# Optimization experiments

Measured on AMD Instinct MI355X. Metric: run time of the kernel, lower is better.

## Reference

```python
import jax, jax.numpy as jnp
import numpy as np

DIM = 512
HID = 2048
E = 16
B = 8
N = 2048
THRESHOLD = 0.8
CAP_FACTOR = 2.0  # eval mode
MIN_EXPERT_CAPACITY = 4
LOSS_COEF = 0.01
CAP = max(MIN_EXPERT_CAPACITY, min(N, int(N * CAP_FACTOR / E)))  # 256


def setup_inputs() -> dict:
    key = jax.random.key(0)
    k1, k2, k3, k4 = jax.random.split(key, 4)
    x = jax.random.normal(k1, (B, N, DIM), dtype=jnp.float32)
    w_gating = jax.random.normal(k2, (DIM, E), dtype=jnp.float32)
    std1 = 1.0 / np.sqrt(HID)
    std2 = 1.0 / np.sqrt(DIM)
    w1 = jax.random.uniform(k3, (E, DIM, HID), jnp.float32, -std1, std1)
    w2 = jax.random.uniform(k4, (E, HID, DIM), jnp.float32, -std2, std2)
    return {"x": x, "w_gating": w_gating, "w1": w1, "w2": w2}


def _gate(x, w_gating):
    # raw gate probabilities [B, N, E]
    raw = jax.nn.softmax(jnp.einsum('bnd,de->bne', x, w_gating), axis=-1)
    order = jnp.argsort(-raw, axis=-1)                      # descending sort indices
    sp = jnp.take_along_axis(raw, order, axis=-1)           # sorted probs (desc)
    cum = jnp.cumsum(sp, axis=-1)
    tm = cum >= THRESHOLD
    k = jnp.argmax(tm.astype(jnp.float32), axis=-1) + 1     # dynamic k per token
    k = jnp.where(jnp.any(tm, axis=-1), k, E)
    # select top-k in sorted order, renormalize
    rank = jnp.arange(E)
    sel = (rank < k[..., None]).astype(raw.dtype)           # [B,N,E] sorted order
    selp = sp * sel
    normp = selp / jnp.sum(selp, axis=-1, keepdims=True)
    # scatter back to expert order via inverse permutation
    inv = jnp.argsort(order, axis=-1)
    mask = jnp.take_along_axis(sel, inv, axis=-1)           # expert_masks [B,N,E]
    weights = jnp.take_along_axis(normp, inv, axis=-1)      # expert_weights
    # capacity: exclusive cumsum over tokens
    pos = (jnp.cumsum(mask, axis=-2) - mask) * mask
    mask = mask * (pos < float(CAP)).astype(mask.dtype)
    pos = pos * mask
    pos_tok = jnp.sum(pos, axis=-1).astype(jnp.int32)       # [B,N] (summed across experts, as in source)
    in_cap = (pos_tok < CAP).astype(raw.dtype)
    oh = jax.nn.one_hot(pos_tok, CAP, dtype=raw.dtype) * in_cap[..., None]  # [B,N,CAP]
    dispatch = mask[..., None] * oh[..., None, :]           # [B,N,E,CAP]
    combine = (weights * mask)[..., None] * oh[..., None, :]
    density = jnp.mean(mask, axis=-2)
    density_proxy = jnp.mean(raw, axis=-2)
    loss = jnp.mean(density_proxy * density) * float(E * E)
    loss = loss + 0.0 * jnp.mean(k.astype(jnp.float32))
    return dispatch, combine, loss


def reference(x, w_gating, w1, w2):
    dispatch, combine, loss = _gate(x, w_gating)
    expert_inputs = jnp.einsum('bnd,bnec->ebcd', x, dispatch)        # [E,B,CAP,D]
    ei = expert_inputs.reshape(E, B * CAP, DIM)
    hidden = jax.nn.gelu(jnp.einsum('end,edh->enh', ei, w1), approximate=False)
    eo = jnp.einsum('enh,ehd->end', hidden, w2).reshape(E, B, CAP, DIM)
    output = jnp.einsum('ebcd,bnec->bnd', eo, combine)               # [B,N,D]
    return output, loss * LOSS_COEF
```

## Files before the change

kernel.cpp:

```cpp
#include <hip/hip_runtime.h>
#include <math.h>

#define DIMC 512
#define HIDC 2048
#define EC   16
#define BC   8
#define NC   2048
#define CAPC 256
#define BN   (BC * NC)
#define THRESH 0.8f

typedef unsigned short u16;
typedef __attribute__((ext_vector_type(8))) __bf16 bf16x8;
typedef __attribute__((ext_vector_type(4))) float f32x4;

__device__ __forceinline__ float bf2f(unsigned u) {
    union { unsigned i; float f; } v; v.i = u << 16; return v.f;
}
__device__ __forceinline__ u16 f2bf(float f) {
    union { float f; unsigned i; } v; v.f = f;
    unsigned r = v.i + 0x7fff + ((v.i >> 16) & 1);
    return (u16)(r >> 16);
}
__device__ __forceinline__ float gelu_f(float x) {
    float u = 0.7978845608028654f * (x + 0.044715f * x * x * x);
    float t = __expf(2.f * u);
    float th = 1.f - 2.f / (t + 1.f);
    return 0.5f * x * (1.f + th);
}

__global__ void init_kernel(int* __restrict__ heads, int* __restrict__ pos_tok)
{
    int i = blockIdx.x * 256 + threadIdx.x;
    if (i < EC * BC * CAPC) heads[i] = -1;
    if (i < BN) pos_tok[i] = 0;
}

__global__ __launch_bounds__(256) void gate_kernel(const float* __restrict__ x,
                                                   const float* __restrict__ wg,
                                                   float* __restrict__ raw,
                                                   float* __restrict__ weights,
                                                   float* __restrict__ maskf)
{
    __shared__ float wlds[16][516];
    __shared__ float lg[16][16];
    int t = threadIdx.x;
    int tok16 = t >> 4, e = t & 15;
    int token = blockIdx.x * 16 + tok16;

    {
        const float4* wg4 = (const float4*)wg;
#pragma unroll
        for (int j = 0; j < 8; ++j) {
            int idx4 = j * 256 + t;
            float4 v = wg4[idx4];
            int d  = idx4 >> 2;
            int e0 = (idx4 & 3) * 4;
            wlds[e0 + 0][d] = v.x;
            wlds[e0 + 1][d] = v.y;
            wlds[e0 + 2][d] = v.z;
            wlds[e0 + 3][d] = v.w;
        }
    }
    __syncthreads();

    const float4* xr = (const float4*)(x + (size_t)token * DIMC);
    const float4* wl = (const float4*)&wlds[e][0];
    float a0 = 0.f, a1 = 0.f, a2 = 0.f, a3 = 0.f;
#pragma unroll 4
    for (int i = 0; i < 128; i += 4) {
        float4 xa = xr[i], xb = xr[i+1], xc = xr[i+2], xd = xr[i+3];
        float4 wa = wl[i], wb = wl[i+1], wc = wl[i+2], wd = wl[i+3];
        a0 = fmaf(xa.w, wa.w, fmaf(xa.z, wa.z, fmaf(xa.y, wa.y, fmaf(xa.x, wa.x, a0))));
        a1 = fmaf(xb.w, wb.w, fmaf(xb.z, wb.z, fmaf(xb.y, wb.y, fmaf(xb.x, wb.x, a1))));
        a2 = fmaf(xc.w, wc.w, fmaf(xc.z, wc.z, fmaf(xc.y, wc.y, fmaf(xc.x, wc.x, a2))));
        a3 = fmaf(xd.w, wd.w, fmaf(xd.z, wd.z, fmaf(xd.y, wd.y, fmaf(xd.x, wd.x, a3))));
    }
    float logit = (a0 + a1) + (a2 + a3);

    float m = logit;
#pragma unroll
    for (int off = 8; off >= 1; off >>= 1) m = fmaxf(m, __shfl_xor(m, off, 16));
    float p = expf(logit - m);
    float s = p;
#pragma unroll
    for (int off = 8; off >= 1; off >>= 1) s += __shfl_xor(s, off, 16);
    p = p / s;

    int rank = 0;
    float cum = p;
#pragma unroll
    for (int j = 1; j < 16; ++j) {
        float op = __shfl_xor(p, j, 16);
        int oidx = e ^ j;
        bool ahead = (op > p) || (op == p && oidx < e);
        if (ahead) { rank++; cum += op; }
    }
    bool tm = (cum >= THRESH);
    int kr = tm ? rank : (EC - 1);
#pragma unroll
    for (int off = 8; off >= 1; off >>= 1) kr = min(kr, __shfl_xor(kr, off, 16));
    bool sel = (rank <= kr);

    float dsel = sel ? p : 0.f;
    float denom = dsel;
#pragma unroll
    for (int off = 8; off >= 1; off >>= 1) denom += __shfl_xor(denom, off, 16);
    float w = sel ? (p / denom) : 0.f;

    size_t o = (size_t)token * EC + e;
    raw[o]     = p;
    weights[o] = w;
    maskf[o]   = sel ? 1.f : 0.f;
    (void)lg;
}

__global__ __launch_bounds__(64) void capacity_kernel(const float* __restrict__ raw,
                                                      float* __restrict__ maskf,
                                                      int* __restrict__ pos,
                                                      int* __restrict__ pos_tok,
                                                      float* __restrict__ density,
                                                      float* __restrict__ proxy)
{
    int t = blockIdx.x;
    int b = t / EC, e = t % EC;
    int lane = threadIdx.x;

    size_t idx = ((size_t)b * NC + lane) * EC + e;
    const size_t step = (size_t)64 * EC;
    float mv = maskf[idx];
    float rv = raw[idx];

    int count = 0;
    float rsum = 0.f;
    for (int n0 = 0; n0 < NC; n0 += 64) {
        float mn = 0.f, rn = 0.f;
        if (n0 + 64 < NC) { mn = maskf[idx + step]; rn = raw[idx + step]; }

        rsum += rv;
        unsigned long long bal = __ballot(mv != 0.f);
        int below = __popcll(bal & ((1ull << lane) - 1ull));
        int pval = 0;
        if (mv != 0.f) {
            pval = count + below;
            if (pval >= CAPC) { maskf[idx] = 0.f; pval = 0; }
            else if (pval > 0) atomicAdd(&pos_tok[b * NC + n0 + lane], pval);
        }
        pos[idx] = pval;
        count += __popcll(bal);

        idx += step; mv = mn; rv = rn;
    }
#pragma unroll
    for (int off = 32; off >= 1; off >>= 1) rsum += __shfl_xor(rsum, off);
    if (lane == 0) {
        int admitted = count < CAPC ? count : CAPC;
        density[t] = (float)admitted / (float)NC;
        proxy[t]   = rsum / (float)NC;
    }
}

__global__ __launch_bounds__(256) void build_kernel(const float* __restrict__ maskf,
                                                    const int* __restrict__ pos,
                                                    const int* __restrict__ pos_tok,
                                                    int* __restrict__ heads,
                                                    int* __restrict__ nxt,
                                                    int* __restrict__ node_tok)
{
    int id = blockIdx.x * 256 + threadIdx.x;
    int token = id >> 4, e = id & 15;
    if (maskf[id] == 0.f) return;
    int c = pos_tok[token];
    if (c >= CAPC) return;
    int b = token >> 11;
    int slot = (e * BC + b) * CAPC + c;
    int node = (e * BC + b) * CAPC + pos[id];
    node_tok[node] = token;
    nxt[node] = atomicExch(&heads[slot], node);
}

__global__ __launch_bounds__(256) void gather_ei_kernel(const float* __restrict__ x,
                                                        const int* __restrict__ heads,
                                                        const int* __restrict__ nxt,
                                                        const int* __restrict__ node_tok,
                                                        u16* __restrict__ ei)
{
    int slot = blockIdx.x * 4 + (threadIdx.x >> 6);
    int lane = threadIdx.x & 63;
    float a[8] = {0,0,0,0,0,0,0,0};
    int node = heads[slot];
    while (node >= 0) {
        const float4* xr = (const float4*)(x + (size_t)node_tok[node] * DIMC) + lane * 2;
        float4 v0 = xr[0], v1 = xr[1];
        a[0]+=v0.x; a[1]+=v0.y; a[2]+=v0.z; a[3]+=v0.w;
        a[4]+=v1.x; a[5]+=v1.y; a[6]+=v1.z; a[7]+=v1.w;
        node = nxt[node];
    }
    uint4 v;
    v.x = (unsigned)f2bf(a[0]) | ((unsigned)f2bf(a[1]) << 16);
    v.y = (unsigned)f2bf(a[2]) | ((unsigned)f2bf(a[3]) << 16);
    v.z = (unsigned)f2bf(a[4]) | ((unsigned)f2bf(a[5]) << 16);
    v.w = (unsigned)f2bf(a[6]) | ((unsigned)f2bf(a[7]) << 16);
    *(uint4*)(ei + (size_t)slot * DIMC + lane * 8) = v;
}

__global__ __launch_bounds__(256) void transpose_cvt_all_kernel(const float* __restrict__ w1,
                                                                const float* __restrict__ w2,
                                                                u16* __restrict__ w1t,
                                                                u16* __restrict__ w2t)
{
    __shared__ float tile[64][65];
    int bid = blockIdx.x;
    const float* in; u16* out; int R, C, bx, by, e;
    if (bid < 4096) {
        e = bid >> 8; int r = bid & 255;
        bx = r & 31; by = r >> 5;
        in = w1; out = w1t; R = DIMC; C = HIDC;
    } else {
        bid -= 4096;
        e = bid >> 8; int r = bid & 255;
        bx = r & 7;  by = r >> 3;
        in = w2; out = w2t; R = HIDC; C = DIMC;
    }
    size_t eoff = (size_t)e * R * C;
    int c0 = bx * 64, r0 = by * 64;
    int tid = threadIdx.x;
    int rr = tid >> 4;
    int cc = (tid & 15) * 4;
#pragma unroll
    for (int i = 0; i < 4; ++i) {
        float4 v = *(const float4*)(in + eoff + (size_t)(r0 + rr + 16 * i) * C + c0 + cc);
        tile[rr + 16 * i][cc + 0] = v.x;
        tile[rr + 16 * i][cc + 1] = v.y;
        tile[rr + 16 * i][cc + 2] = v.z;
        tile[rr + 16 * i][cc + 3] = v.w;
    }
    __syncthreads();
    int c = tid >> 2;
    int r8 = (tid & 3) * 16;
    u16 buf[16];
#pragma unroll
    for (int j = 0; j < 16; ++j) buf[j] = f2bf(tile[r8 + j][c]);
    u16* op = out + eoff + (size_t)(c0 + c) * R + r0 + r8;
    *(uint4*)(op)     = *(uint4*)&buf[0];
    *(uint4*)(op + 8) = *(uint4*)&buf[8];
}

__device__ __forceinline__ void async_cp16(const u16* g, u16* l) {
    __builtin_amdgcn_global_load_lds(
        (const __attribute__((address_space(1))) unsigned*)g,
        (__attribute__((address_space(3))) unsigned*)l, 16, 0, 0);
}

#define GFENCE() asm volatile("" ::: "memory")
#define BAR() do { GFENCE(); __builtin_amdgcn_s_barrier(); GFENCE(); } while (0)

__device__ __forceinline__ int xcd_swz(int id, int nwg) {
    int chunk = nwg >> 3;
    return (id & 7) * chunk + (id >> 3);
}

template<int GELU>
__global__ __launch_bounds__(512, 2) void gemm256_kernel(
    const u16* __restrict__ A, const u16* __restrict__ Bt, u16* __restrict__ C,
    int M, int N, int K, long sA, long sB, long sC)
{
    __shared__ __align__(16) u16 lds[2][2][2][8192];
    const int bxc = N >> 8, byc = M >> 8;
    int swzid = xcd_swz(blockIdx.x, gridDim.x);
    const int e  = swzid / (bxc * byc);
    int rr2 = swzid % (bxc * byc);
    const int bm = (rr2 / bxc) * 256, bn = (rr2 % bxc) * 256;
    const int t = threadIdx.x, lane = t & 63, w = t >> 6;
    const int wm = w & 1;
    const int wn = w >> 1;
    const int bh = wn >> 1;
    const int q = lane >> 4, m16 = lane & 15;

    const u16* g[2][2][2];
    int lofs[2];
#pragma unroll
    for (int j = 0; j < 2; ++j) {
        int l = j * 512 + t, r = l >> 3, c = (l & 7) ^ (r & 7);
        lofs[j] = l * 8;
        g[0][0][j] = A  + (size_t)e * sA + (size_t)(bm + r) * K + c * 8;
        g[0][1][j] = A  + (size_t)e * sA + (size_t)(bm + 128 + r) * K + c * 8;
        g[1][0][j] = Bt + (size_t)e * sB + (size_t)(bn + r) * K + c * 8;
        g[1][1][j] = Bt + (size_t)e * sB + (size_t)(bn + 128 + r) * K + c * 8;
    }

    int aro[8], bro[4];
#pragma unroll
    for (int mt = 0; mt < 8; ++mt) {
        int r = mt * 16 + m16;
        aro[mt] = r * 64 + (q ^ (r & 7)) * 8;
    }
#pragma unroll
    for (int nt = 0; nt < 4; ++nt) {
        int r = (wn & 1) * 64 + nt * 16 + m16;
        bro[nt] = r * 64 + (q ^ (r & 7)) * 8;
    }

    auto STAGE = [&](int buf, int op, int half) {
#pragma unroll
        for (int j = 0; j < 2; ++j) {
            async_cp16(g[op][half][j], &lds[buf][op][half][lofs[j]]);
            g[op][half][j] += 64;
        }
    };

    const int nk = K >> 6;
    STAGE(0, 1, 0); STAGE(0, 1, 1);
    STAGE(0, 0, 0); STAGE(0, 0, 1);
    if (nk > 1) {
        STAGE(1, 1, 0); STAGE(1, 1, 1);
        asm volatile("s_waitcnt vmcnt(4)" ::: "memory");
    } else {
        asm volatile("s_waitcnt vmcnt(0)" ::: "memory");
    }
    BAR();

    f32x4 acc[8][4] = {};
    for (int ti = 0; ti < nk; ++ti) {
        const int cur = ti & 1, nx = cur ^ 1;
        const u16* lA = &lds[cur][0][wm][0];
        const u16* lB = &lds[cur][1][bh][0];
        bf16x8 a0[4][2], a1[4][2], b01[2][2], b23[2][2];

#pragma unroll
        for (int mt = 0; mt < 4; ++mt)
#pragma unroll
            for (int kk = 0; kk < 2; ++kk)
                a0[mt][kk] = *(const bf16x8*)&lA[aro[mt] ^ (kk * 32)];
#pragma unroll
        for (int nt = 0; nt < 2; ++nt)
#pragma unroll
            for (int kk = 0; kk < 2; ++kk)
                b01[nt][kk] = *(const bf16x8*)&lB[bro[nt] ^ (kk * 32)];
        if (ti + 1 < nk) STAGE(nx, 0, 0);
        BAR();
        asm volatile("s_waitcnt lgkmcnt(0)" ::: "memory");
        __builtin_amdgcn_s_setprio(1);
#pragma unroll
        for (int mt = 0; mt < 4; ++mt)
#pragma unroll
            for (int nt = 0; nt < 2; ++nt)
#pragma unroll
                for (int kk = 0; kk < 2; ++kk)
                    acc[mt][nt] = __builtin_amdgcn_mfma_f32_16x16x32_bf16(
                        a0[mt][kk], b01[nt][kk], acc[mt][nt], 0, 0, 0);
        __builtin_amdgcn_s_setprio(0);
        BAR();

#pragma unroll
        for (int nt = 0; nt < 2; ++nt)
#pragma unroll
            for (int kk = 0; kk < 2; ++kk)
                b23[nt][kk] = *(const bf16x8*)&lB[bro[2 + nt] ^ (kk * 32)];
        if (ti + 1 < nk) STAGE(nx, 0, 1);
        BAR();
        asm volatile("s_waitcnt lgkmcnt(0)" ::: "memory");
        __builtin_amdgcn_s_setprio(1);
#pragma unroll
        for (int mt = 0; mt < 4; ++mt)
#pragma unroll
            for (int nt = 0; nt < 2; ++nt)
#pragma unroll
                for (int kk = 0; kk < 2; ++kk)
                    acc[mt][2 + nt] = __builtin_amdgcn_mfma_f32_16x16x32_bf16(
                        a0[mt][kk], b23[nt][kk], acc[mt][2 + nt], 0, 0, 0);
        __builtin_amdgcn_s_setprio(0);
        BAR();

#pragma unroll
        for (int mt = 0; mt < 4; ++mt)
#pragma unroll
            for (int kk = 0; kk < 2; ++kk)
                a1[mt][kk] = *(const bf16x8*)&lA[aro[4 + mt] ^ (kk * 32)];
        if (ti + 2 < nk) STAGE(cur, 1, 0);
        BAR();
        asm volatile("s_waitcnt lgkmcnt(0)" ::: "memory");
        __builtin_amdgcn_s_setprio(1);
#pragma unroll
        for (int mt = 0; mt < 4; ++mt)
#pragma unroll
            for (int nt = 0; nt < 2; ++nt)
#pragma unroll
                for (int kk = 0; kk < 2; ++kk)
                    acc[4 + mt][2 + nt] = __builtin_amdgcn_mfma_f32_16x16x32_bf16(
                        a1[mt][kk], b23[nt][kk], acc[4 + mt][2 + nt], 0, 0, 0);
        __builtin_amdgcn_s_setprio(0);
        BAR();

        if (ti + 2 < nk) STAGE(cur, 1, 1);
        BAR();
        __builtin_amdgcn_s_setprio(1);
#pragma unroll
        for (int mt = 0; mt < 4; ++mt)
#pragma unroll
            for (int nt = 0; nt < 2; ++nt)
#pragma unroll
                for (int kk = 0; kk < 2; ++kk)
                    acc[4 + mt][nt] = __builtin_amdgcn_mfma_f32_16x16x32_bf16(
                        a1[mt][kk], b01[nt][kk], acc[4 + mt][nt], 0, 0, 0);
        __builtin_amdgcn_s_setprio(0);
        if (ti + 1 < nk) {
            if (ti + 2 < nk) asm volatile("s_waitcnt vmcnt(4)" ::: "memory");
            else             asm volatile("s_waitcnt vmcnt(0)" ::: "memory");
        }
        BAR();
    }

    const size_t cbase = (size_t)e * sC;
#pragma unroll
    for (int mt = 0; mt < 8; ++mt)
#pragma unroll
        for (int nt = 0; nt < 4; ++nt)
#pragma unroll
            for (int r2 = 0; r2 < 4; ++r2) {
                int row = bm + wm * 128 + mt * 16 + q * 4 + r2;
                int col = bn + wn * 64 + nt * 16 + m16;
                float v = acc[mt][nt][r2];
                if (GELU) v = gelu_f(v);
                C[cbase + (size_t)row * N + col] = f2bf(v);
            }
}

__global__ __launch_bounds__(512, 2) void gemm_ffn2_kernel(
    const u16* __restrict__ A, const u16* __restrict__ Bt, u16* __restrict__ C,
    int N, int K, long sA, long sB, long sC)
{
    __shared__ __align__(16) u16 lds[2][3][8192];
    const int bxc = N >> 8, byc = 2048 >> 7;
    int swzid = xcd_swz(blockIdx.x, gridDim.x);
    const int e  = swzid / (bxc * byc);
    int rr2 = swzid % (bxc * byc);
    const int bm = (rr2 / bxc) * 128, bn = (rr2 % bxc) * 256;
    const int t = threadIdx.x, lane = t & 63, w = t >> 6;
    const int wm = w & 1, wn = w >> 1;
    const int bh = wn >> 1;
    const int q = lane >> 4, m16 = lane & 15;

    const u16* gA[2]; const u16* gB[2][2];
    int lofs[2];
#pragma unroll
    for (int j = 0; j < 2; ++j) {
        int l = j * 512 + t, r = l >> 3, c = (l & 7) ^ (r & 7);
        lofs[j] = l * 8;
        gA[j]    = A  + (size_t)e * sA + (size_t)(bm + r) * K + c * 8;
        gB[0][j] = Bt + (size_t)e * sB + (size_t)(bn + r) * K + c * 8;
        gB[1][j] = Bt + (size_t)e * sB + (size_t)(bn + 128 + r) * K + c * 8;
    }

    int aro[4], bro[4];
#pragma unroll
    for (int mt = 0; mt < 4; ++mt) {
        int r = wm * 64 + mt * 16 + m16;
        aro[mt] = r * 64 + (q ^ (r & 7)) * 8;
    }
#pragma unroll
    for (int nt = 0; nt < 4; ++nt) {
        int r = (wn & 1) * 64 + nt * 16 + m16;
        bro[nt] = r * 64 + (q ^ (r & 7)) * 8;
    }

    auto STAGE_A = [&](int buf) {
#pragma unroll
        for (int j = 0; j < 2; ++j) { async_cp16(gA[j], &lds[buf][0][lofs[j]]); gA[j] += 64; }
    };
    auto STAGE_B = [&](int buf, int half) {
#pragma unroll
        for (int j = 0; j < 2; ++j) { async_cp16(gB[half][j], &lds[buf][1 + half][lofs[j]]); gB[half][j] += 64; }
    };

    const int nk = K >> 6;
    STAGE_A(0); STAGE_B(0, 0); STAGE_B(0, 1);
    if (nk > 1) {
        STAGE_B(1, 0); STAGE_B(1, 1);
        asm volatile("s_waitcnt vmcnt(4)" ::: "memory");
    } else {
        asm volatile("s_waitcnt vmcnt(0)" ::: "memory");
    }
    BAR();

    f32x4 acc[4][4] = {};
    for (int ti = 0; ti < nk; ++ti) {
        const int cur = ti & 1, nx = cur ^ 1;
        const u16* lA = &lds[cur][0][0];
        const u16* lB = &lds[cur][1 + bh][0];
        bf16x8 a01[2][2], a23[2][2], b01[2][2], b23[2][2];

#pragma unroll
        for (int mt = 0; mt < 2; ++mt)
#pragma unroll
            for (int kk = 0; kk < 2; ++kk)
                a01[mt][kk] = *(const bf16x8*)&lA[aro[mt] ^ (kk * 32)];
#pragma unroll
        for (int nt = 0; nt < 2; ++nt)
#pragma unroll
            for (int kk = 0; kk < 2; ++kk)
                b01[nt][kk] = *(const bf16x8*)&lB[bro[nt] ^ (kk * 32)];
        if (ti + 1 < nk) STAGE_A(nx);
        BAR();
        asm volatile("s_waitcnt lgkmcnt(0)" ::: "memory");
        __builtin_amdgcn_s_setprio(1);
#pragma unroll
        for (int mt = 0; mt < 2; ++mt)
#pragma unroll
            for (int nt = 0; nt < 2; ++nt)
#pragma unroll
                for (int kk = 0; kk < 2; ++kk)
                    acc[mt][nt] = __builtin_amdgcn_mfma_f32_16x16x32_bf16(
                        a01[mt][kk], b01[nt][kk], acc[mt][nt], 0, 0, 0);
        __builtin_amdgcn_s_setprio(0);
        BAR();

#pragma unroll
        for (int nt = 0; nt < 2; ++nt)
#pragma unroll
            for (int kk = 0; kk < 2; ++kk)
                b23[nt][kk] = *(const bf16x8*)&lB[bro[2 + nt] ^ (kk * 32)];
        BAR();
        asm volatile("s_waitcnt lgkmcnt(0)" ::: "memory");
        __builtin_amdgcn_s_setprio(1);
#pragma unroll
        for (int mt = 0; mt < 2; ++mt)
#pragma unroll
            for (int nt = 0; nt < 2; ++nt)
#pragma unroll
                for (int kk = 0; kk < 2; ++kk)
                    acc[mt][2 + nt] = __builtin_amdgcn_mfma_f32_16x16x32_bf16(
                        a01[mt][kk], b23[nt][kk], acc[mt][2 + nt], 0, 0, 0);
        __builtin_amdgcn_s_setprio(0);
        BAR();

#pragma unroll
        for (int mt = 0; mt < 2; ++mt)
#pragma unroll
            for (int kk = 0; kk < 2; ++kk)
                a23[mt][kk] = *(const bf16x8*)&lA[aro[2 + mt] ^ (kk * 32)];
        if (ti + 2 < nk) STAGE_B(cur, 0);
        BAR();
        asm volatile("s_waitcnt lgkmcnt(0)" ::: "memory");
        __builtin_amdgcn_s_setprio(1);
#pragma unroll
        for (int mt = 0; mt < 2; ++mt)
#pragma unroll
            for (int nt = 0; nt < 2; ++nt)
#pragma unroll
                for (int kk = 0; kk < 2; ++kk)
                    acc[2 + mt][2 + nt] = __builtin_amdgcn_mfma_f32_16x16x32_bf16(
                        a23[mt][kk], b23[nt][kk], acc[2 + mt][2 + nt], 0, 0, 0);
        __builtin_amdgcn_s_setprio(0);
        BAR();

        if (ti + 2 < nk) STAGE_B(cur, 1);
        BAR();
        __builtin_amdgcn_s_setprio(1);
#pragma unroll
        for (int mt = 0; mt < 2; ++mt)
#pragma unroll
            for (int nt = 0; nt < 2; ++nt)
#pragma unroll
                for (int kk = 0; kk < 2; ++kk)
                    acc[2 + mt][nt] = __builtin_amdgcn_mfma_f32_16x16x32_bf16(
                        a23[mt][kk], b01[nt][kk], acc[2 + mt][nt], 0, 0, 0);
        __builtin_amdgcn_s_setprio(0);
        if (ti + 1 < nk) {
            if (ti + 2 < nk) asm volatile("s_waitcnt vmcnt(4)" ::: "memory");
            else             asm volatile("s_waitcnt vmcnt(0)" ::: "memory");
        }
        BAR();
    }

    const size_t cbase = (size_t)e * sC;
#pragma unroll
    for (int mt = 0; mt < 4; ++mt)
#pragma unroll
        for (int nt = 0; nt < 4; ++nt)
#pragma unroll
            for (int r2 = 0; r2 < 4; ++r2) {
                int row = bm + wm * 64 + mt * 16 + q * 4 + r2;
                int col = bn + wn * 64 + nt * 16 + m16;
                C[cbase + (size_t)row * N + col] = f2bf(acc[mt][nt][r2]);
            }
}

__global__ __launch_bounds__(256) void combine_kernel(const u16* __restrict__ eo,
                                                      const float* __restrict__ weights,
                                                      const float* __restrict__ maskf,
                                                      const int* __restrict__ pos_tok,
                                                      float* __restrict__ out)
{
    int token = blockIdx.x;
    int tid   = threadIdx.x;
    int b = token >> 11;
    int c = pos_tok[token];
    float a0 = 0.f, a1 = 0.f;
    if (c < CAPC) {
        const float* wr = weights + (size_t)token * EC;
        const float* mr = maskf   + (size_t)token * EC;
#pragma unroll
        for (int e = 0; e < EC; ++e) {
            float wm = wr[e] * mr[e];
            if (wm != 0.f) {
                const u16* src = eo + (((size_t)e * BC + b) * CAPC + c) * DIMC;
                unsigned u = *(const unsigned*)(src + 2 * tid);
                a0 += wm * bf2f(u & 0xffffu);
                a1 += wm * bf2f(u >> 16);
            }
        }
    }
    *(float2*)(out + (size_t)token * DIMC + 2 * tid) = make_float2(a0, a1);
}

__global__ void loss_kernel(const float* __restrict__ density,
                            const float* __restrict__ proxy,
                            float* __restrict__ out_loss)
{
    __shared__ float sh[BC * EC];
    int t = threadIdx.x;
    sh[t] = density[t] * proxy[t];
    __syncthreads();
    for (int s2 = (BC * EC) / 2; s2 >= 1; s2 >>= 1) {
        if (t < s2) sh[t] += sh[t + s2];
        __syncthreads();
    }
    if (t == 0)
        out_loss[0] = sh[0] * ((float)(EC * EC) / (float)(BC * EC)) * 0.01f;
}

extern "C" void kernel_launch(void* const* d_in, const int* in_sizes, int n_in,
                              void* d_out, int out_size, void* d_ws, size_t ws_size,
                              hipStream_t stream)
{
    const float* x  = (const float*)d_in[0];
    const float* wg = (const float*)d_in[1];
    const float* w1 = (const float*)d_in[2];
    const float* w2 = (const float*)d_in[3];
    float* out = (float*)d_out;

    char* ws = (char*)d_ws;
    size_t off = 0;
    auto alloc = [&](size_t bytes) -> void* {
        void* p = ws + off;
        off = (off + bytes + 255) & ~(size_t)255;
        return p;
    };
    float* raw      = (float*)alloc((size_t)BN * EC * 4);
    float* weights  = (float*)alloc((size_t)BN * EC * 4);
    float* maskf    = (float*)alloc((size_t)BN * EC * 4);
    int*   pos      = (int*)  alloc((size_t)BN * EC * 4);
    int*   pos_tok  = (int*)  alloc((size_t)BN * 4);
    int*   heads    = (int*)  alloc((size_t)EC * BC * CAPC * 4);
    int*   nxt      = (int*)  alloc((size_t)EC * BC * CAPC * 4);
    int*   node_tok = (int*)  alloc((size_t)EC * BC * CAPC * 4);
    float* density  = (float*)alloc(BC * EC * 4);
    float* proxy    = (float*)alloc(BC * EC * 4);
    u16*   ei_bf    = (u16*)alloc((size_t)EC * BC * CAPC * DIMC * 2);
    u16*   w1t      = (u16*)alloc((size_t)EC * DIMC * HIDC * 2);
    u16*   w2t      = (u16*)alloc((size_t)EC * HIDC * DIMC * 2);
    u16*   eo_bf    = (u16*)alloc((size_t)EC * BC * CAPC * DIMC * 2);
    size_t hid_full = (size_t)EC * BC * CAPC * HIDC * 2;
    int ngroups = (ws_size - off >= hid_full) ? 1 : 2;
    int EG = EC / ngroups;
    u16* hidden = (u16*)alloc((size_t)EG * BC * CAPC * HIDC * 2);

    (void)in_sizes; (void)n_in; (void)out_size;

    init_kernel<<<(EC * BC * CAPC + 255) / 256, 256, 0, stream>>>(heads, pos_tok);
    transpose_cvt_all_kernel<<<8192, 256, 0, stream>>>(w1, w2, w1t, w2t);

    gate_kernel<<<BN / 16, 256, 0, stream>>>(x, wg, raw, weights, maskf);
    capacity_kernel<<<BC * EC, 64, 0, stream>>>(raw, maskf, pos, pos_tok, density, proxy);
    build_kernel<<<BN * EC / 256, 256, 0, stream>>>(maskf, pos, pos_tok, heads, nxt, node_tok);
    gather_ei_kernel<<<EC * BC * CAPC / 4, 256, 0, stream>>>(x, heads, nxt, node_tok, ei_bf);

    for (int g = 0; g < ngroups; ++g) {
        const u16* Ag  = ei_bf + (size_t)g * EG * BC * CAPC * DIMC;
        const u16* B1g = w1t   + (size_t)g * EG * DIMC * HIDC;
        gemm256_kernel<1><<<(HIDC / 256) * ((BC * CAPC) / 256) * EG, 512, 0, stream>>>(
            Ag, B1g, hidden, BC * CAPC, HIDC, DIMC,
            (long)BC * CAPC * DIMC, (long)HIDC * DIMC, (long)BC * CAPC * HIDC);
        const u16* B2g = w2t + (size_t)g * EG * HIDC * DIMC;
        u16* Eg = eo_bf + (size_t)g * EG * BC * CAPC * DIMC;
        gemm_ffn2_kernel<<<(DIMC / 256) * ((BC * CAPC) / 128) * EG, 512, 0, stream>>>(
            hidden, B2g, Eg, DIMC, HIDC,
            (long)BC * CAPC * HIDC, (long)DIMC * HIDC, (long)BC * CAPC * DIMC);
    }

    combine_kernel<<<BN, 256, 0, stream>>>(eo_bf, weights, maskf, pos_tok, out);
    loss_kernel<<<1, BC * EC, 0, stream>>>(density, proxy, out + (size_t)BN * DIMC);
}
```

Before: 445.5 us.

## Fuse gating with weight transpose and merge capacity/build into per-batch route kernel

Merges the gate and weight transpose/convert kernels into a single launch. Replaces the init, capacity and build kernels with one per-batch block that computes positions, per-token offsets and the slot linked lists in shared memory, using only shared-memory atomics. Folds the loss reduction into the gather kernel. This cuts launch count and global atomic traffic, but the routing step now runs on only 8 large blocks, which reduces parallelism.

Measured after the change: 461.7 us. +3.6%, slower.

```diff
diff --git a/kernel.cpp b/kernel.cpp
--- a/kernel.cpp
+++ b/kernel.cpp
@@ -29,108 +29,149 @@
     return 0.5f * x * (1.f + th);
 }
 
-__global__ void init_kernel(int* __restrict__ heads, int* __restrict__ pos_tok)
+__global__ __launch_bounds__(256) void front_kernel(const float* __restrict__ x,
+                                                    const float* __restrict__ wg,
+                                                    const float* __restrict__ w1,
+                                                    const float* __restrict__ w2,
+                                                    float* __restrict__ raw,
+                                                    float* __restrict__ weights,
+                                                    float* __restrict__ maskf,
+                                                    u16* __restrict__ w1t,
+                                                    u16* __restrict__ w2t)
 {
-    int i = blockIdx.x * 256 + threadIdx.x;
-    if (i < EC * BC * CAPC) heads[i] = -1;
-    if (i < BN) pos_tok[i] = 0;
-}
-
-__global__ __launch_bounds__(256) void gate_kernel(const float* __restrict__ x,
-                                                   const float* __restrict__ wg,
-                                                   float* __restrict__ raw,
-                                                   float* __restrict__ weights,
-                                                   float* __restrict__ maskf)
+    __shared__ float smem[16 * 516];
+    int bid = blockIdx.x;
+    int t = threadIdx.x;
+
+    if (bid < 1024) {
+        float (*wlds)[516] = (float(*)[516])smem;
+        int tok16 = t >> 4, e = t & 15;
+        int token = bid * 16 + tok16;
+        {
+            const float4* wg4 = (const float4*)wg;
+#pragma unroll
+            for (int j = 0; j < 8; ++j) {
+                int idx4 = j * 256 + t;
+                float4 v = wg4[idx4];
+                int d  = idx4 >> 2;
+                int e0 = (idx4 & 3) * 4;
+                wlds[e0 + 0][d] = v.x;
+                wlds[e0 + 1][d] = v.y;
+                wlds[e0 + 2][d] = v.z;
+                wlds[e0 + 3][d] = v.w;
+            }
+        }
+        __syncthreads();
+
+        const float4* xr = (const float4*)(x + (size_t)token * DIMC);
+        const float4* wl = (const float4*)&wlds[e][0];
+        float a0 = 0.f, a1 = 0.f, a2 = 0.f, a3 = 0.f;
+#pragma unroll 4
+        for (int i = 0; i < 128; i += 4) {
+            float4 xa = xr[i], xb = xr[i+1], xc = xr[i+2], xd = xr[i+3];
+            float4 wa = wl[i], wb = wl[i+1], wc = wl[i+2], wd = wl[i+3];
+            a0 = fmaf(xa.w, wa.w, fmaf(xa.z, wa.z, fmaf(xa.y, wa.y, fmaf(xa.x, wa.x, a0))));
+            a1 = fmaf(xb.w, wb.w, fmaf(xb.z, wb.z, fmaf(xb.y, wb.y, fmaf(xb.x, wb.x, a1))));
+            a2 = fmaf(xc.w, wc.w, fmaf(xc.z, wc.z, fmaf(xc.y, wc.y, fmaf(xc.x, wc.x, a2))));
+            a3 = fmaf(xd.w, wd.w, fmaf(xd.z, wd.z, fmaf(xd.y, wd.y, fmaf(xd.x, wd.x, a3))));
+        }
+        float logit = (a0 + a1) + (a2 + a3);
+
+        float m = logit;
+#pragma unroll
+        for (int off = 8; off >= 1; off >>= 1) m = fmaxf(m, __shfl_xor(m, off, 16));
+        float p = expf(logit - m);
+        float s = p;
+#pragma unroll
+        for (int off = 8; off >= 1; off >>= 1) s += __shfl_xor(s, off, 16);
+        p = p / s;
+
+        int rank = 0;
+        float cum = p;
+#pragma unroll
+        for (int j = 1; j < 16; ++j) {
+            float op = __shfl_xor(p, j, 16);
+            int oidx = e ^ j;
+            bool ahead = (op > p) || (op == p && oidx < e);
+            if (ahead) { rank++; cum += op; }
+        }
+        bool tm = (cum >= THRESH);
+        int kr = tm ? rank : (EC - 1);
+#pragma unroll
+        for (int off = 8; off >= 1; off >>= 1) kr = min(kr, __shfl_xor(kr, off, 16));
+        bool sel = (rank <= kr);
+
+        float dsel = sel ? p : 0.f;
+        float denom = dsel;
+#pragma unroll
+        for (int off = 8; off >= 1; off >>= 1) denom += __shfl_xor(denom, off, 16);
+        float w = sel ? (p / denom) : 0.f;
+
+        size_t o = (size_t)token * EC + e;
+        raw[o]     = p;
+        weights[o] = w;
+        maskf[o]   = sel ? 1.f : 0.f;
+        return;
+    }
+
+    float (*tile)[65] = (float(*)[65])smem;
+    int bid2 = bid - 1024;
+    const float* in; u16* out; int R, C, bx, by, e;
+    if (bid2 < 4096) {
+        e = bid2 >> 8; int r = bid2 & 255;
+        bx = r & 31; by = r >> 5;
+        in = w1; out = w1t; R = DIMC; C = HIDC;
+    } else {
+        bid2 -= 4096;
+        e = bid2 >> 8; int r = bid2 & 255;
+        bx = r & 7;  by = r >> 3;
+        in = w2; out = w2t; R = HIDC; C = DIMC;
+    }
+    size_t eoff = (size_t)e * R * C;
+    int c0 = bx * 64, r0 = by * 64;
+    int rr = t >> 4;
+    int cc = (t & 15) * 4;
+#pragma unroll
+    for (int i = 0; i < 4; ++i) {
+        float4 v = *(const float4*)(in + eoff + (size_t)(r0 + rr + 16 * i) * C + c0 + cc);
+        tile[rr + 16 * i][cc + 0] = v.x;
+        tile[rr + 16 * i][cc + 1] = v.y;
+        tile[rr + 16 * i][cc + 2] = v.z;
+        tile[rr + 16 * i][cc + 3] = v.w;
+    }
+    __syncthreads();
+    int c = t >> 2;
+    int r8 = (t & 3) * 16;
+    u16 buf[16];
+#pragma unroll
+    for (int j = 0; j < 16; ++j) buf[j] = f2bf(tile[r8 + j][c]);
+    u16* op = out + eoff + (size_t)(c0 + c) * R + r0 + r8;
+    *(uint4*)(op)     = *(uint4*)&buf[0];
+    *(uint4*)(op + 8) = *(uint4*)&buf[8];
+}
+
+__global__ __launch_bounds__(1024) void route_kernel(const float* __restrict__ raw,
+                                                     float* __restrict__ maskf,
+                                                     int* __restrict__ pos_tok_g,
+                                                     int* __restrict__ heads,
+                                                     int* __restrict__ nxt,
+                                                     int* __restrict__ node_tok,
+                                                     float* __restrict__ density,
+                                                     float* __restrict__ proxy)
 {
-    __shared__ float wlds[16][516];
-    __shared__ float lg[16][16];
-    int t = threadIdx.x;
-    int tok16 = t >> 4, e = t & 15;
-    int token = blockIdx.x * 16 + tok16;
-
-    {
-        const float4* wg4 = (const float4*)wg;
-#pragma unroll
-        for (int j = 0; j < 8; ++j) {
-            int idx4 = j * 256 + t;
-            float4 v = wg4[idx4];
-            int d  = idx4 >> 2;
-            int e0 = (idx4 & 3) * 4;
-            wlds[e0 + 0][d] = v.x;
-            wlds[e0 + 1][d] = v.y;
-            wlds[e0 + 2][d] = v.z;
-            wlds[e0 + 3][d] = v.w;
-        }
-    }
-    __syncthreads();
-
-    const float4* xr = (const float4*)(x + (size_t)token * DIMC);
-    const float4* wl = (const float4*)&wlds[e][0];
-    float a0 = 0.f, a1 = 0.f, a2 = 0.f, a3 = 0.f;
-#pragma unroll 4
-    for (int i = 0; i < 128; i += 4) {
-        float4 xa = xr[i], xb = xr[i+1], xc = xr[i+2], xd = xr[i+3];
-        float4 wa = wl[i], wb = wl[i+1], wc = wl[i+2], wd = wl[i+3];
-        a0 = fmaf(xa.w, wa.w, fmaf(xa.z, wa.z, fmaf(xa.y, wa.y, fmaf(xa.x, wa.x, a0))));
-        a1 = fmaf(xb.w, wb.w, fmaf(xb.z, wb.z, fmaf(xb.y, wb.y, fmaf(xb.x, wb.x, a1))));
-        a2 = fmaf(xc.w, wc.w, fmaf(xc.z, wc.z, fmaf(xc.y, wc.y, fmaf(xc.x, wc.x, a2))));
-        a3 = fmaf(xd.w, wd.w, fmaf(xd.z, wd.z, fmaf(xd.y, wd.y, fmaf(xd.x, wd.x, a3))));
-    }
-    float logit = (a0 + a1) + (a2 + a3);
-
-    float m = logit;
-#pragma unroll
-    for (int off = 8; off >= 1; off >>= 1) m = fmaxf(m, __shfl_xor(m, off, 16));
-    float p = expf(logit - m);
-    float s = p;
-#pragma unroll
-    for (int off = 8; off >= 1; off >>= 1) s += __shfl_xor(s, off, 16);
-    p = p / s;
-
-    int rank = 0;
-    float cum = p;
-#pragma unroll
-    for (int j = 1; j < 16; ++j) {
-        float op = __shfl_xor(p, j, 16);
-        int oidx = e ^ j;
-        bool ahead = (op > p) || (op == p && oidx < e);
-        if (ahead) { rank++; cum += op; }
-    }
-    bool tm = (cum >= THRESH);
-    int kr = tm ? rank : (EC - 1);
-#pragma unroll
-    for (int off = 8; off >= 1; off >>= 1) kr = min(kr, __shfl_xor(kr, off, 16));
-    bool sel = (rank <= kr);
-
-    float dsel = sel ? p : 0.f;
-    float denom = dsel;
-#pragma unroll
-    for (int off = 8; off >= 1; off >>= 1) denom += __shfl_xor(denom, off, 16);
-    float w = sel ? (p / denom) : 0.f;
-
-    size_t o = (size_t)token * EC + e;
-    raw[o]     = p;
-    weights[o] = w;
-    maskf[o]   = sel ? 1.f : 0.f;
-    (void)lg;
-}
-
-__global__ __launch_bounds__(64) void capacity_kernel(const float* __restrict__ raw,
-                                                      float* __restrict__ maskf,
-                                                      int* __restrict__ pos,
-                                                      int* __restrict__ pos_tok,
-                                                      float* __restrict__ density,
-                                                      float* __restrict__ proxy)
-{
-    int t = blockIdx.x;
-    int b = t / EC, e = t % EC;
-    int lane = threadIdx.x;
+    __shared__ u16 posl[NC][EC];
+    __shared__ int headsl[EC][CAPC];
+    __shared__ u16 ptok[NC];
+    const int b = blockIdx.x;
+    const int tid = threadIdx.x;
+    const int e = tid >> 6, lane = tid & 63;
+
+    for (int i = tid; i < EC * CAPC; i += 1024) ((int*)headsl)[i] = -1;
 
     size_t idx = ((size_t)b * NC + lane) * EC + e;
     const size_t step = (size_t)64 * EC;
     float mv = maskf[idx];
     float rv = raw[idx];
-
     int count = 0;
     float rsum = 0.f;
     for (int n0 = 0; n0 < NC; n0 += 64) {
@@ -140,13 +181,13 @@
         rsum += rv;
         unsigned long long bal = __ballot(mv != 0.f);
         int below = __popcll(bal & ((1ull << lane) - 1ull));
-        int pval = 0;
+        int pp = 0;
         if (mv != 0.f) {
-            pval = count + below;
-            if (pval >= CAPC) { maskf[idx] = 0.f; pval = 0; }
-            else if (pval > 0) atomicAdd(&pos_tok[b * NC + n0 + lane], pval);
-        }
-        pos[idx] = pval;
+            int pval = count + below;
+            if (pval >= CAPC) maskf[idx] = 0.f;
+            else pp = pval + 1;
+        }
+        posl[n0 + lane][e] = (u16)pp;
         count += __popcll(bal);
 
         idx += step; mv = mn; rv = rn;
@@ -155,36 +196,63 @@
     for (int off = 32; off >= 1; off >>= 1) rsum += __shfl_xor(rsum, off);
     if (lane == 0) {
         int admitted = count < CAPC ? count : CAPC;
-        density[t] = (float)admitted / (float)NC;
-        proxy[t]   = rsum / (float)NC;
-    }
-}
-
-__global__ __launch_bounds__(256) void build_kernel(const float* __restrict__ maskf,
-                                                    const int* __restrict__ pos,
-                                                    const int* __restrict__ pos_tok,
-                                                    int* __restrict__ heads,
-                                                    int* __restrict__ nxt,
-                                                    int* __restrict__ node_tok)
+        density[b * EC + e] = (float)admitted / (float)NC;
+        proxy[b * EC + e]   = rsum / (float)NC;
+    }
+    __syncthreads();
+
+    for (int n = tid; n < NC; n += 1024) {
+        int s = 0;
+#pragma unroll
+        for (int ee = 0; ee < EC; ++ee) {
+            int v = posl[n][ee];
+            s += (v > 0) ? (v - 1) : 0;
+        }
+        ptok[n] = (u16)s;
+        pos_tok_g[b * NC + n] = s;
+    }
+    __syncthreads();
+
+    for (int i = tid; i < NC * EC; i += 1024) {
+        int n = i >> 4, ee = i & 15;
+        int pp = posl[n][ee];
+        if (pp == 0) continue;
+        int c = ptok[n];
+        if (c >= CAPC) continue;
+        int node = (ee * BC + b) * CAPC + (pp - 1);
+        node_tok[node] = b * NC + n;
+        nxt[node] = atomicExch(&headsl[ee][c], node);
+    }
+    __syncthreads();
+
+    for (int i = tid; i < EC * CAPC; i += 1024) {
+        int ee = i >> 8, c = i & 255;
+        heads[(ee * BC + b) * CAPC + c] = headsl[ee][c];
+    }
+}
+
+__global__ __launch_bounds__(256) void gather_loss_kernel(const float* __restrict__ x,
+                                                          const int* __restrict__ heads,
+                                                          const int* __restrict__ nxt,
+                                                          const int* __restrict__ node_tok,
+                                                          u16* __restrict__ ei,
+                                                          const float* __restrict__ density,
+                                                          const float* __restrict__ proxy,
+                                                          float* __restrict__ out_loss)
 {
-    int id = blockIdx.x * 256 + threadIdx.x;
-    int token = id >> 4, e = id & 15;
-    if (maskf[id] == 0.f) return;
-    int c = pos_tok[token];
-    if (c >= CAPC) return;
-    int b = token >> 11;
-    int slot = (e * BC + b) * CAPC + c;
-    int node = (e * BC + b) * CAPC + pos[id];
-    node_tok[node] = token;
-    nxt[node] = atomicExch(&heads[slot], node);
-}
-
-__global__ __launch_bounds__(256) void gather_ei_kernel(const float* __restrict__ x,
-                                                        const int* __restrict__ heads,
-                                                        const int* __restrict__ nxt,
-                                                        const int* __restrict__ node_tok,
-                                                        u16* __restrict__ ei)
-{
+    if (blockIdx.x == 8192) {
+        __shared__ float sh[BC * EC];
+        int t = threadIdx.x;
+        if (t < BC * EC) sh[t] = density[t] * proxy[t];
+        __syncthreads();
+        for (int s2 = (BC * EC) / 2; s2 >= 1; s2 >>= 1) {
+            if (t < s2) sh[t] += sh[t + s2];
+            __syncthreads();
+        }
+        if (t == 0)
+            out_loss[0] = sh[0] * ((float)(EC * EC) / (float)(BC * EC)) * 0.01f;
+        return;
+    }
     int slot = blockIdx.x * 4 + (threadIdx.x >> 6);
     int lane = threadIdx.x & 63;
     float a[8] = {0,0,0,0,0,0,0,0};
@@ -202,48 +270,6 @@
     v.z = (unsigned)f2bf(a[4]) | ((unsigned)f2bf(a[5]) << 16);
     v.w = (unsigned)f2bf(a[6]) | ((unsigned)f2bf(a[7]) << 16);
     *(uint4*)(ei + (size_t)slot * DIMC + lane * 8) = v;
-}
-
-__global__ __launch_bounds__(256) void transpose_cvt_all_kernel(const float* __restrict__ w1,
-                                                                const float* __restrict__ w2,
-                                                                u16* __restrict__ w1t,
-                                                                u16* __restrict__ w2t)
-{
-    __shared__ float tile[64][65];
-    int bid = blockIdx.x;
-    const float* in; u16* out; int R, C, bx, by, e;
-    if (bid < 4096) {
-        e = bid >> 8; int r = bid & 255;
-        bx = r & 31; by = r >> 5;
-        in = w1; out = w1t; R = DIMC; C = HIDC;
-    } else {
-        bid -= 4096;
-        e = bid >> 8; int r = bid & 255;
-        bx = r & 7;  by = r >> 3;
-        in = w2; out = w2t; R = HIDC; C = DIMC;
-    }
-    size_t eoff = (size_t)e * R * C;
-    int c0 = bx * 64, r0 = by * 64;
-    int tid = threadIdx.x;
-    int rr = tid >> 4;
-    int cc = (tid & 15) * 4;
-#pragma unroll
-    for (int i = 0; i < 4; ++i) {
-        float4 v = *(const float4*)(in + eoff + (size_t)(r0 + rr + 16 * i) * C + c0 + cc);
-        tile[rr + 16 * i][cc + 0] = v.x;
-        tile[rr + 16 * i][cc + 1] = v.y;
-        tile[rr + 16 * i][cc + 2] = v.z;
-        tile[rr + 16 * i][cc + 3] = v.w;
-    }
-    __syncthreads();
-    int c = tid >> 2;
-    int r8 = (tid & 3) * 16;
-    u16 buf[16];
-#pragma unroll
-    for (int j = 0; j < 16; ++j) buf[j] = f2bf(tile[r8 + j][c]);
-    u16* op = out + eoff + (size_t)(c0 + c) * R + r0 + r8;
-    *(uint4*)(op)     = *(uint4*)&buf[0];
-    *(uint4*)(op + 8) = *(uint4*)&buf[8];
 }
 
 __device__ __forceinline__ void async_cp16(const u16* g, u16* l) {
@@ -614,22 +640,6 @@
     *(float2*)(out + (size_t)token * DIMC + 2 * tid) = make_float2(a0, a1);
 }
 
-__global__ void loss_kernel(const float* __restrict__ density,
-                            const float* __restrict__ proxy,
-                            float* __restrict__ out_loss)
-{
-    __shared__ float sh[BC * EC];
-    int t = threadIdx.x;
-    sh[t] = density[t] * proxy[t];
-    __syncthreads();
-    for (int s2 = (BC * EC) / 2; s2 >= 1; s2 >>= 1) {
-        if (t < s2) sh[t] += sh[t + s2];
-        __syncthreads();
-    }
-    if (t == 0)
-        out_loss[0] = sh[0] * ((float)(EC * EC) / (float)(BC * EC)) * 0.01f;
-}
-
 extern "C" void kernel_launch(void* const* d_in, const int* in_sizes, int n_in,
                               void* d_out, int out_size, void* d_ws, size_t ws_size,
                               hipStream_t stream)
@@ -650,7 +660,6 @@
     float* raw      = (float*)alloc((size_t)BN * EC * 4);
     float* weights  = (float*)alloc((size_t)BN * EC * 4);
     float* maskf    = (float*)alloc((size_t)BN * EC * 4);
-    int*   pos      = (int*)  alloc((size_t)BN * EC * 4);
     int*   pos_tok  = (int*)  alloc((size_t)BN * 4);
     int*   heads    = (int*)  alloc((size_t)EC * BC * CAPC * 4);
     int*   nxt      = (int*)  alloc((size_t)EC * BC * CAPC * 4);
@@ -668,13 +677,12 @@
 
     (void)in_sizes; (void)n_in; (void)out_size;
 
-    init_kernel<<<(EC * BC * CAPC + 255) / 256, 256, 0, stream>>>(heads, pos_tok);
-    transpose_cvt_all_kernel<<<8192, 256, 0, stream>>>(w1, w2, w1t, w2t);
-
-    gate_kernel<<<BN / 16, 256, 0, stream>>>(x, wg, raw, weights, maskf);
-    capacity_kernel<<<BC * EC, 64, 0, stream>>>(raw, maskf, pos, pos_tok, density, proxy);
-    build_kernel<<<BN * EC / 256, 256, 0, stream>>>(maskf, pos, pos_tok, heads, nxt, node_tok);
-    gather_ei_kernel<<<EC * BC * CAPC / 4, 256, 0, stream>>>(x, heads, nxt, node_tok, ei_bf);
+    front_kernel<<<1024 + 8192, 256, 0, stream>>>(x, wg, w1, w2,
+                                                  raw, weights, maskf, w1t, w2t);
+    route_kernel<<<BC, 1024, 0, stream>>>(raw, maskf, pos_tok,
+                                          heads, nxt, node_tok, density, proxy);
+    gather_loss_kernel<<<EC * BC * CAPC / 4 + 1, 256, 0, stream>>>(
+        x, heads, nxt, node_tok, ei_bf, density, proxy, out + (size_t)BN * DIMC);
 
     for (int g = 0; g < ngroups; ++g) {
         const u16* Ag  = ei_bf + (size_t)g * EG * BC * CAPC * DIMC;
@@ -690,5 +698,4 @@
     }
 
     combine_kernel<<<BN, 256, 0, stream>>>(eo_bf, weights, maskf, pos_tok, out);
-    loss_kernel<<<1, BC * EC, 0, stream>>>(density, proxy, out + (size_t)BN * DIMC);
-}
+}
```
